# Kernel optimization log

Measured on AMD Instinct MI355X. Metric: run time of the kernel, lower is better.

The kernel has to match this reference:

```python
import jax, jax.numpy as jnp
import numpy as np

N = 100000   # nodes
E = 1600000  # edges (avg degree 16)
DIM = 128    # feature dim
EPS = 1e-6
NEG_SLOPE = 0.2  # tf.nn.leaky_relu default alpha


def layernorm(x, g, b):
    m = jnp.mean(x, axis=-1, keepdims=True)
    v = jnp.mean(jnp.square(x - m), axis=-1, keepdims=True)
    return g * (x - m) * jax.lax.rsqrt(v + EPS) + b


def setup_inputs() -> dict:
    key = jax.random.key(0)
    ks = jax.random.split(key, 12)
    s = 1.0 / np.sqrt(DIM)
    return {
        "query": jax.random.normal(ks[0], (N, DIM), jnp.float32),
        "adj_val": jax.random.uniform(ks[1], (E,), jnp.float32),
        "w_W": jax.random.normal(ks[2], (DIM, DIM), jnp.float32) * s,
        "w_b": jnp.zeros((DIM,), jnp.float32),
        "w1_W": jax.random.normal(ks[3], (DIM, DIM), jnp.float32) * s,
        "w1_b": jnp.zeros((DIM,), jnp.float32),
        "w2_W": jax.random.normal(ks[4], (DIM, DIM), jnp.float32) * s,
        "w2_b": jnp.zeros((DIM,), jnp.float32),
        "ln1_g": jnp.ones((DIM,), jnp.float32),
        "ln1_b": jnp.zeros((DIM,), jnp.float32),
        "ln2_g": jnp.ones((DIM,), jnp.float32),
        "ln2_b": jnp.zeros((DIM,), jnp.float32),
        "adj_row": jnp.sort(jax.random.randint(ks[5], (E,), 0, N, jnp.int32)),
        "adj_col": jax.random.randint(ks[6], (E,), 0, N, jnp.int32),
    }


def reference(query, adj_val, w_W, w_b, w1_W, w1_b, w2_W, w2_b,
              ln1_g, ln1_b, ln2_g, ln2_b, adj_row, adj_col):
    q = layernorm(query, ln1_g, ln1_b)          # [N, D]
    k = q                                        # key is None -> key = query
    value = k @ w_W + w_b                        # [N, D]

    # per-node scalar scores (mean_sum=False branch); dropout in eval mode (identity)
    sum1 = jnp.tanh(jnp.sum(q @ w1_W + w1_b, axis=1))   # [N]
    sum2 = jnp.tanh(jnp.sum(k @ w2_W + w2_b, axis=1))   # [N]

    # sparse add of col-scaled and row-scaled adjacency, then leaky_relu
    logits = jax.nn.leaky_relu(
        adj_val * sum1[adj_row] + adj_val * sum2[adj_col], NEG_SLOPE)  # [E]

    # sparse row-wise softmax over nonzeros
    row_max = jax.ops.segment_max(logits, adj_row, num_segments=N)
    ex = jnp.exp(logits - row_max[adj_row])
    row_sum = jax.ops.segment_sum(ex, adj_row, num_segments=N)
    attn = ex / row_sum[adj_row]                 # [E]

    # spmm: out[i] = sum_e attn[e] * value[col[e]]
    out = jax.ops.segment_sum(attn[:, None] * value[adj_col], adj_row,
                              num_segments=N)    # [N, D]
    return layernorm(out, ln2_g, ln2_b)
```

## Files before the change

### kernel.cpp

```cpp
#include <hip/hip_runtime.h>
#include <hip/hip_bf16.h>

typedef __attribute__((ext_vector_type(8))) short short8;
typedef __attribute__((ext_vector_type(8))) unsigned short ushort8;
typedef __attribute__((ext_vector_type(4))) float f32x4;
typedef __attribute__((ext_vector_type(2))) float f32x2;
typedef __attribute__((ext_vector_type(4))) unsigned int uint4v;

#define DIM 128
#define EPS 1e-6f

__device__ __forceinline__ float wave_sum(float v){
  #pragma unroll
  for (int m = 32; m >= 1; m >>= 1) v += __shfl_xor(v, m);
  return v;
}

__global__ void setup_kernel(const float* __restrict__ w_W,
                             const float* __restrict__ w1_W, const float* __restrict__ w1_b,
                             const float* __restrict__ w2_W, const float* __restrict__ w2_b,
                             __hip_bfloat16* __restrict__ wt_bf,
                             float* __restrict__ u1, float* __restrict__ u2,
                             float* __restrict__ c12){
  const int b = blockIdx.x, tid = threadIdx.x;
  if (b == 0){
    __shared__ float p1s[256], p2s[256];
    const int d = tid & 127, half = tid >> 7;
    const float4* w1p = (const float4*)(w1_W + d*DIM + half*64);
    const float4* w2p = (const float4*)(w2_W + d*DIM + half*64);
    float s1 = 0.f, s2 = 0.f;
    #pragma unroll 4
    for (int j = 0; j < 16; ++j){
      float4 a = w1p[j]; s1 += (a.x + a.y) + (a.z + a.w);
      float4 c = w2p[j]; s2 += (c.x + c.y) + (c.z + c.w);
    }
    p1s[tid] = s1; p2s[tid] = s2;
    __syncthreads();
    if (tid < 128){ u1[tid] = p1s[tid] + p1s[tid+128]; u2[tid] = p2s[tid] + p2s[tid+128]; }
    if (tid < 64){
      float c1 = w1_b[tid] + w1_b[tid + 64];
      float c2 = w2_b[tid] + w2_b[tid + 64];
      c1 = wave_sum(c1); c2 = wave_sum(c2);
      if (tid == 0){ c12[0] = c1; c12[1] = c2; }
    }
  } else {
    int idx = (b - 1) * 256 + tid;
    int j = idx >> 7, d = idx & 127;
    wt_bf[idx] = __float2bfloat16(w_W[d*DIM + j]);
  }
}

__launch_bounds__(256)
__global__ void node_kernel(const float* __restrict__ query,
                            const __hip_bfloat16* __restrict__ wt_bf,
                            const float* __restrict__ w_b,
                            const float* __restrict__ ln1_g, const float* __restrict__ ln1_b,
                            const float* __restrict__ u1, const float* __restrict__ u2,
                            const float* __restrict__ c12,
                            unsigned char* __restrict__ value_q,
                            float* __restrict__ sum1, float2* __restrict__ s2v, int N){
  __shared__ __hip_bfloat16 A[64][136];
  const int tid  = threadIdx.x;
  const int lane = tid & 63;
  const int w    = tid >> 6;
  const int q16  = lane >> 4;
  const int lq   = lane & 15;
  const int base = blockIdx.x * 64;

  float uu1[8], uu2[8], gg[8], bv[8];
  {
    const float* p1 = u1 + lq*8; const float* p2 = u2 + lq*8;
    const float* pg = ln1_g + lq*8; const float* pb = ln1_b + lq*8;
    #pragma unroll
    for (int j = 0; j < 8; ++j){ uu1[j]=p1[j]; uu2[j]=p2[j]; gg[j]=pg[j]; bv[j]=pb[j]; }
  }
  const float c1 = c12[0], c2 = c12[1];

  #pragma unroll
  for (int it = 0; it < 4; ++it){
    const int row = w*16 + it*4 + q16;
    const int n   = base + row;
    float x[8];
    if (n < N){
      const float4* qp = (const float4*)(query + (size_t)n*DIM + lq*8);
      float4 a = qp[0], b = qp[1];
      x[0]=a.x; x[1]=a.y; x[2]=a.z; x[3]=a.w;
      x[4]=b.x; x[5]=b.y; x[6]=b.z; x[7]=b.w;
    } else {
      #pragma unroll
      for (int j = 0; j < 8; ++j) x[j] = 0.f;
    }
    float s = 0.f, s2 = 0.f;
    #pragma unroll
    for (int j = 0; j < 8; ++j){ s += x[j]; s2 += x[j]*x[j]; }
    #pragma unroll
    for (int m = 1; m <= 8; m <<= 1){ s += __shfl_xor(s, m); s2 += __shfl_xor(s2, m); }
    const float mean = s * (1.f/128.f);
    const float var  = s2 * (1.f/128.f) - mean*mean;
    const float rs   = rsqrtf(var + EPS);

    float p1 = 0.f, p2 = 0.f;
    unsigned pk[4];
    #pragma unroll
    for (int j = 0; j < 4; ++j){
      float n0 = gg[2*j]   * (x[2*j]   - mean) * rs + bv[2*j];
      float n1 = gg[2*j+1] * (x[2*j+1] - mean) * rs + bv[2*j+1];
      p1 += n0*uu1[2*j] + n1*uu1[2*j+1];
      p2 += n0*uu2[2*j] + n1*uu2[2*j+1];
      union { __hip_bfloat16 h; unsigned short u; } a_, b_;
      a_.h = __float2bfloat16(n0); b_.h = __float2bfloat16(n1);
      pk[j] = ((unsigned)b_.u << 16) | (unsigned)a_.u;
    }
    uint4v pv = { pk[0], pk[1], pk[2], pk[3] };
    *(uint4v*)&A[row][lq*8] = pv;
    #pragma unroll
    for (int m = 1; m <= 8; m <<= 1){ p1 += __shfl_xor(p1, m); p2 += __shfl_xor(p2, m); }
    if (lq == 0 && n < N){
      sum1[n]   = tanhf(p1 + c1);
      s2v[n].x  = tanhf(p2 + c2);
    }
  }
  __syncthreads();

  const int rh = (w & 1) * 32;
  const int ch = (w >> 1) * 64;
  short8 afr[2][4];
  #pragma unroll
  for (int m = 0; m < 2; ++m)
    #pragma unroll
    for (int ks = 0; ks < 4; ++ks)
      afr[m][ks] = *(const short8*)&A[rh + m*16 + lq][ks*32 + q16*8];
  __syncthreads();

  #pragma unroll
  for (int jj = 0; jj < 4; ++jj){
    const int colb = ch + jj*16;
    f32x4 acc[2];
    acc[0] = (f32x4){0.f,0.f,0.f,0.f};
    acc[1] = (f32x4){0.f,0.f,0.f,0.f};
    #pragma unroll
    for (int ks = 0; ks < 4; ++ks){
      short8 bfr = *(const short8*)(wt_bf + (size_t)(colb + lq)*DIM + ks*32 + q16*8);
      acc[0] = __builtin_amdgcn_mfma_f32_16x16x32_bf16(afr[0][ks], bfr, acc[0], 0, 0, 0);
      acc[1] = __builtin_amdgcn_mfma_f32_16x16x32_bf16(afr[1][ks], bfr, acc[1], 0, 0, 0);
    }
    const int col  = colb + lq;
    const float bias = w_b[col];
    #pragma unroll
    for (int m = 0; m < 2; ++m)
      #pragma unroll
      for (int i = 0; i < 4; ++i)
        A[rh + m*16 + q16*4 + i][col] = __float2bfloat16(acc[m][i] + bias);
  }
  __syncthreads();

  const int row = tid >> 2, seg = tid & 3;
  const int n = base + row;
  float vals[32];
  float amax = 0.f;
  const ushort8* ap = (const ushort8*)&A[row][seg*32];
  #pragma unroll
  for (int h = 0; h < 4; ++h){
    ushort8 vv = ap[h];
    #pragma unroll
    for (int j = 0; j < 8; ++j){
      float f = __uint_as_float((unsigned)vv[j] << 16);
      vals[h*8 + j] = f;
      amax = fmaxf(amax, fabsf(f));
    }
  }
  amax = fmaxf(amax, __shfl_xor(amax, 1));
  amax = fmaxf(amax, __shfl_xor(amax, 2));
  const float qs = amax > 0.f ? 127.f / amax : 0.f;
  if (n < N){
    if (seg == 0) s2v[n].y = amax * (1.f/127.f);
    unsigned dw[8];
    #pragma unroll
    for (int d = 0; d < 8; ++d){
      unsigned q0 = (unsigned)__float2int_rn(fmaf(vals[4*d+0], qs, 128.f));
      unsigned q1 = (unsigned)__float2int_rn(fmaf(vals[4*d+1], qs, 128.f));
      unsigned q2 = (unsigned)__float2int_rn(fmaf(vals[4*d+2], qs, 128.f));
      unsigned q3 = (unsigned)__float2int_rn(fmaf(vals[4*d+3], qs, 128.f));
      dw[d] = q0 | (q1 << 8) | (q2 << 16) | (q3 << 24);
    }
    uint4v* dst = (uint4v*)(value_q + (size_t)n*DIM + seg*32);
    dst[0] = (uint4v){dw[0], dw[1], dw[2], dw[3]};
    dst[1] = (uint4v){dw[4], dw[5], dw[6], dw[7]};
  }
}

__global__ void pack_kernel(const float* __restrict__ adj_val, const int* __restrict__ adj_row,
                            const int* __restrict__ adj_col,
                            const float* __restrict__ sum1, const float2* __restrict__ s2v,
                            float2* __restrict__ excol, int* __restrict__ row_ptr,
                            int N, int E){
  int e = blockIdx.x * 256 + threadIdx.x;
  if (e >= E) return;
  int r  = adj_row[e];
  int rp = (e > 0) ? adj_row[e-1] : -1;
  if (rp != r){
    for (int rr = rp + 1; rr <= r; ++rr) row_ptr[rr] = e;
  }
  if (e == E - 1){
    for (int rr = r + 1; rr <= N; ++rr) row_ptr[rr] = E;
  }
  float av = adj_val[e];
  int c = adj_col[e];
  float2 sv = s2v[c];
  float x = av * (sum1[r] + sv.x);
  float lg = x > 0.f ? x : 0.2f * x;
  excol[e] = make_float2(__expf(lg) * sv.y, __int_as_float(c << 7));
}

__launch_bounds__(256)
__global__ void edge_kernel(const float2* __restrict__ excol, const int* __restrict__ row_ptr,
                            const unsigned char* __restrict__ value_q,
                            const float* __restrict__ ln2_g, const float* __restrict__ ln2_b,
                            float* __restrict__ out, int N){
  const int lane = threadIdx.x & 63;
  const int half = lane >> 5;
  const int ll   = lane & 31;
  const int q2   = ll >> 4;
  const int lq   = ll & 15;
  const int r = blockIdx.x * 8 + (threadIdx.x >> 6) * 2 + half;
  if (r >= N) return;
  const int2 rp = *(const int2*)(row_ptr + r);
  const int e0 = rp.x, e1 = rp.y;
  const unsigned char* vbase = value_q + lq*8;

  f32x2 acc2[4];
  #pragma unroll
  for (int j = 0; j < 4; ++j) acc2[j] = (f32x2){0.f, 0.f};

  int sb = e0;
  for (; sb + 8 <= e1; sb += 8){
    #pragma unroll
    for (int t = 0; t < 4; ++t){
      float2 ecv = excol[sb + q2 + t*2];
      const float wsc = ecv.x;
      const unsigned voff = (unsigned)__float_as_int(ecv.y);
      uint2 v = *(const uint2*)(vbase + voff);
      f32x2 w2 = { wsc, wsc };
      f32x2 p0 = { (float)( v.x        & 0xff), (float)((v.x >>  8) & 0xff) };
      f32x2 p1 = { (float)((v.x >> 16) & 0xff), (float)( v.x >> 24)         };
      f32x2 p2 = { (float)( v.y        & 0xff), (float)((v.y >>  8) & 0xff) };
      f32x2 p3 = { (float)((v.y >> 16) & 0xff), (float)( v.y >> 24)         };
      acc2[0] += w2 * p0;
      acc2[1] += w2 * p1;
      acc2[2] += w2 * p2;
      acc2[3] += w2 * p3;
    }
  }
  if (sb < e1){
    #pragma unroll
    for (int t = 0; t < 4; ++t){
      const int e = sb + q2 + t*2;
      float2 ecv = (e < e1) ? excol[e] : make_float2(0.f, 0.f);
      const float wsc = ecv.x;
      const unsigned voff = (unsigned)__float_as_int(ecv.y);
      uint2 v = *(const uint2*)(vbase + voff);
      f32x2 w2 = { wsc, wsc };
      f32x2 p0 = { (float)( v.x        & 0xff), (float)((v.x >>  8) & 0xff) };
      f32x2 p1 = { (float)((v.x >> 16) & 0xff), (float)( v.x >> 24)         };
      f32x2 p2 = { (float)( v.y        & 0xff), (float)((v.y >>  8) & 0xff) };
      f32x2 p3 = { (float)((v.y >> 16) & 0xff), (float)( v.y >> 24)         };
      acc2[0] += w2 * p0;
      acc2[1] += w2 * p1;
      acc2[2] += w2 * p2;
      acc2[3] += w2 * p3;
    }
  }

  #pragma unroll
  for (int j = 0; j < 4; ++j){
    acc2[j].x += __shfl_xor(acc2[j].x, 16);
    acc2[j].y += __shfl_xor(acc2[j].y, 16);
  }

  float sx = 0.f, sxx = 0.f;
  #pragma unroll
  for (int j = 0; j < 4; ++j){
    sx  += acc2[j].x + acc2[j].y;
    sxx += acc2[j].x*acc2[j].x + acc2[j].y*acc2[j].y;
  }
  #pragma unroll
  for (int m = 1; m <= 8; m <<= 1){ sx += __shfl_xor(sx, m); sxx += __shfl_xor(sxx, m); }
  const float mean = sx * (1.f/128.f);
  const float var  = sxx * (1.f/128.f) - mean*mean;
  const float rs   = rsqrtf(var + EPS);

  if (q2 == 0){
    float4 g0 = ((const float4*)ln2_g)[lq*2], g1 = ((const float4*)ln2_g)[lq*2+1];
    float4 b0 = ((const float4*)ln2_b)[lq*2], b1 = ((const float4*)ln2_b)[lq*2+1];
    float4 o0, o1;
    o0.x = g0.x*(acc2[0].x-mean)*rs + b0.x; o0.y = g0.y*(acc2[0].y-mean)*rs + b0.y;
    o0.z = g0.z*(acc2[1].x-mean)*rs + b0.z; o0.w = g0.w*(acc2[1].y-mean)*rs + b0.w;
    o1.x = g1.x*(acc2[2].x-mean)*rs + b1.x; o1.y = g1.y*(acc2[2].y-mean)*rs + b1.y;
    o1.z = g1.z*(acc2[3].x-mean)*rs + b1.z; o1.w = g1.w*(acc2[3].y-mean)*rs + b1.w;
    float4* op = (float4*)(out + (size_t)r*DIM + lq*8);
    op[0] = o0; op[1] = o1;
  }
}

extern "C" void kernel_launch(void* const* d_in, const int* in_sizes, int n_in,
                              void* d_out, int out_size, void* d_ws, size_t ws_size,
                              hipStream_t stream){
  const float* query   = (const float*)d_in[0];
  const float* adj_val = (const float*)d_in[1];
  const float* w_W     = (const float*)d_in[2];
  const float* w_b     = (const float*)d_in[3];
  const float* w1_W    = (const float*)d_in[4];
  const float* w1_b    = (const float*)d_in[5];
  const float* w2_W    = (const float*)d_in[6];
  const float* w2_b    = (const float*)d_in[7];
  const float* ln1_g   = (const float*)d_in[8];
  const float* ln1_b   = (const float*)d_in[9];
  const float* ln2_g   = (const float*)d_in[10];
  const float* ln2_b   = (const float*)d_in[11];
  const int*   adj_row = (const int*)d_in[12];
  const int*   adj_col = (const int*)d_in[13];

  const int N = in_sizes[0] / DIM;
  const int E = in_sizes[1];

  char* ws = (char*)d_ws;
  size_t off = 0;
  unsigned char* value_q = (unsigned char*)(ws + off); off += (size_t)N * DIM;
  float* sum1   = (float*)(ws + off); off += (size_t)N * 4;
  float2* s2v   = (float2*)(ws + off); off += (size_t)N * 8;
  int* row_ptr  = (int*)(ws + off);   off += (size_t)(N + 2) * 4;
  float* u1     = (float*)(ws + off); off += DIM * 4;
  float* u2     = (float*)(ws + off); off += DIM * 4;
  float* c12    = (float*)(ws + off); off += 2 * 4;
  off = (off + 63) & ~(size_t)63;
  __hip_bfloat16* wt_bf = (__hip_bfloat16*)(ws + off); off += DIM * DIM * 2;
  off = (off + 63) & ~(size_t)63;
  float2* excol = (float2*)(ws + off);

  setup_kernel<<<65, 256, 0, stream>>>(w_W, w1_W, w1_b, w2_W, w2_b, wt_bf, u1, u2, c12);
  node_kernel<<<(N + 63) / 64, 256, 0, stream>>>(query, wt_bf, w_b, ln1_g, ln1_b,
                                                 u1, u2, c12, value_q, sum1, s2v, N);
  pack_kernel<<<(E + 255) / 256, 256, 0, stream>>>(adj_val, adj_row, adj_col,
                                                   sum1, s2v, excol, row_ptr, N, E);
  edge_kernel<<<(N + 7) / 8, 256, 0, stream>>>(excol, row_ptr, value_q,
                                               ln2_g, ln2_b, (float*)d_out, N);
}
```

Before: 93.13 us.

## Fuse edge logit computation into SpMM kernel and build row_ptr by binary search

Removes the separate pack kernel and its intermediate excol array. Edge weights are now computed inside the edge kernel from adj_val, adj_col and the per-node scores. row_ptr is built in the setup kernel by a binary search over adj_row for each row. The change also splits the two tanh evaluations across two lanes and spreads the final LayerNorm stores over both half-waves. This saves one launch and an E-sized write-then-read round trip, at the cost of an extra dependent gather of s2v inside the SpMM loop and of recomputing exp there.

```diff
diff --git a/kernel.cpp b/kernel.cpp
--- a/kernel.cpp
+++ b/kernel.cpp
@@ -19,9 +19,11 @@
 __global__ void setup_kernel(const float* __restrict__ w_W,
                              const float* __restrict__ w1_W, const float* __restrict__ w1_b,
                              const float* __restrict__ w2_W, const float* __restrict__ w2_b,
+                             const int* __restrict__ adj_row,
                              __hip_bfloat16* __restrict__ wt_bf,
                              float* __restrict__ u1, float* __restrict__ u2,
-                             float* __restrict__ c12){
+                             float* __restrict__ c12,
+                             int* __restrict__ row_ptr, int N, int E){
   const int b = blockIdx.x, tid = threadIdx.x;
   if (b == 0){
     __shared__ float p1s[256], p2s[256];
@@ -43,10 +45,17 @@
       c1 = wave_sum(c1); c2 = wave_sum(c2);
       if (tid == 0){ c12[0] = c1; c12[1] = c2; }
     }
-  } else {
+  } else if (b <= 64){
     int idx = (b - 1) * 256 + tid;
     int j = idx >> 7, d = idx & 127;
     wt_bf[idx] = __float2bfloat16(w_W[d*DIM + j]);
+  } else {
+    int r = (b - 65) * 256 + tid;
+    if (r <= N){
+      int lo = 0, hi = E;
+      while (lo < hi){ int mid = (lo + hi) >> 1; if (adj_row[mid] < r) lo = mid + 1; else hi = mid; }
+      row_ptr[r] = lo;
+    }
   }
 }
 
@@ -115,9 +124,11 @@
     *(uint4v*)&A[row][lq*8] = pv;
     #pragma unroll
     for (int m = 1; m <= 8; m <<= 1){ p1 += __shfl_xor(p1, m); p2 += __shfl_xor(p2, m); }
-    if (lq == 0 && n < N){
-      sum1[n]   = tanhf(p1 + c1);
-      s2v[n].x  = tanhf(p2 + c2);
+    if (lq < 2 && n < N){
+      const float arg = (lq == 0) ? (p1 + c1) : (p2 + c2);
+      const float th = tanhf(arg);
+      if (lq == 0) sum1[n] = th;
+      else        s2v[n].x = th;
     }
   }
   __syncthreads();
@@ -189,34 +200,13 @@
   }
 }
 
-__global__ void pack_kernel(const float* __restrict__ adj_val, const int* __restrict__ adj_row,
-                            const int* __restrict__ adj_col,
+__launch_bounds__(256)
+__global__ void edge_kernel(const float* __restrict__ adj_val, const int* __restrict__ adj_col,
+                            const int* __restrict__ row_ptr,
                             const float* __restrict__ sum1, const float2* __restrict__ s2v,
-                            float2* __restrict__ excol, int* __restrict__ row_ptr,
-                            int N, int E){
-  int e = blockIdx.x * 256 + threadIdx.x;
-  if (e >= E) return;
-  int r  = adj_row[e];
-  int rp = (e > 0) ? adj_row[e-1] : -1;
-  if (rp != r){
-    for (int rr = rp + 1; rr <= r; ++rr) row_ptr[rr] = e;
-  }
-  if (e == E - 1){
-    for (int rr = r + 1; rr <= N; ++rr) row_ptr[rr] = E;
-  }
-  float av = adj_val[e];
-  int c = adj_col[e];
-  float2 sv = s2v[c];
-  float x = av * (sum1[r] + sv.x);
-  float lg = x > 0.f ? x : 0.2f * x;
-  excol[e] = make_float2(__expf(lg) * sv.y, __int_as_float(c << 7));
-}
-
-__launch_bounds__(256)
-__global__ void edge_kernel(const float2* __restrict__ excol, const int* __restrict__ row_ptr,
                             const unsigned char* __restrict__ value_q,
                             const float* __restrict__ ln2_g, const float* __restrict__ ln2_b,
-                            float* __restrict__ out, int N){
+                            float* __restrict__ out, int N, int E){
   const int lane = threadIdx.x & 63;
   const int half = lane >> 5;
   const int ll   = lane & 31;
@@ -226,6 +216,7 @@
   if (r >= N) return;
   const int2 rp = *(const int2*)(row_ptr + r);
   const int e0 = rp.x, e1 = rp.y;
+  const float s1r = sum1[r];
   const unsigned char* vbase = value_q + lq*8;
 
   f32x2 acc2[4];
@@ -236,10 +227,14 @@
   for (; sb + 8 <= e1; sb += 8){
     #pragma unroll
     for (int t = 0; t < 4; ++t){
-      float2 ecv = excol[sb + q2 + t*2];
-      const float wsc = ecv.x;
-      const unsigned voff = (unsigned)__float_as_int(ecv.y);
-      uint2 v = *(const uint2*)(vbase + voff);
+      const int e  = sb + q2 + t*2;
+      const float av = adj_val[e];
+      const int   ck = adj_col[e];
+      const float2 sv = s2v[ck];
+      uint2 v = *(const uint2*)(vbase + ((unsigned)ck << 7));
+      const float x   = av * (s1r + sv.x);
+      const float lg  = x > 0.f ? x : 0.2f * x;
+      const float wsc = __expf(lg) * sv.y;
       f32x2 w2 = { wsc, wsc };
       f32x2 p0 = { (float)( v.x        & 0xff), (float)((v.x >>  8) & 0xff) };
       f32x2 p1 = { (float)((v.x >> 16) & 0xff), (float)( v.x >> 24)         };
@@ -254,11 +249,15 @@
   if (sb < e1){
     #pragma unroll
     for (int t = 0; t < 4; ++t){
-      const int e = sb + q2 + t*2;
-      float2 ecv = (e < e1) ? excol[e] : make_float2(0.f, 0.f);
-      const float wsc = ecv.x;
-      const unsigned voff = (unsigned)__float_as_int(ecv.y);
-      uint2 v = *(const uint2*)(vbase + voff);
+      const int e  = sb + q2 + t*2;
+      const int ee = min(e, E - 1);
+      const float av = adj_val[ee];
+      const int   ck = adj_col[ee];
+      const float2 sv = s2v[ck];
+      uint2 v = *(const uint2*)(vbase + ((unsigned)ck << 7));
+      const float x   = av * (s1r + sv.x);
+      const float lg  = x > 0.f ? x : 0.2f * x;
+      const float wsc = (e < e1) ? __expf(lg) * sv.y : 0.f;
       f32x2 w2 = { wsc, wsc };
       f32x2 p0 = { (float)( v.x        & 0xff), (float)((v.x >>  8) & 0xff) };
       f32x2 p1 = { (float)((v.x >> 16) & 0xff), (float)( v.x >> 24)         };
@@ -283,23 +282,23 @@
     sx  += acc2[j].x + acc2[j].y;
     sxx += acc2[j].x*acc2[j].x + acc2[j].y*acc2[j].y;
   }
+  sx *= 0.5f; sxx *= 0.5f;
   #pragma unroll
   for (int m = 1; m <= 8; m <<= 1){ sx += __shfl_xor(sx, m); sxx += __shfl_xor(sxx, m); }
-  const float mean = sx * (1.f/128.f);
-  const float var  = sxx * (1.f/128.f) - mean*mean;
+  const float mean = sx * (2.f/128.f);
+  const float var  = sxx * (2.f/128.f) - mean*mean;
   const float rs   = rsqrtf(var + EPS);
 
-  if (q2 == 0){
-    float4 g0 = ((const float4*)ln2_g)[lq*2], g1 = ((const float4*)ln2_g)[lq*2+1];
-    float4 b0 = ((const float4*)ln2_b)[lq*2], b1 = ((const float4*)ln2_b)[lq*2+1];
-    float4 o0, o1;
-    o0.x = g0.x*(acc2[0].x-mean)*rs + b0.x; o0.y = g0.y*(acc2[0].y-mean)*rs + b0.y;
-    o0.z = g0.z*(acc2[1].x-mean)*rs + b0.z; o0.w = g0.w*(acc2[1].y-mean)*rs + b0.w;
-    o1.x = g1.x*(acc2[2].x-mean)*rs + b1.x; o1.y = g1.y*(acc2[2].y-mean)*rs + b1.y;
-    o1.z = g1.z*(acc2[3].x-mean)*rs + b1.z; o1.w = g1.w*(acc2[3].y-mean)*rs + b1.w;
-    float4* op = (float4*)(out + (size_t)r*DIM + lq*8);
-    op[0] = o0; op[1] = o1;
-  }
+  const float4 gq = ((const float4*)ln2_g)[lq*2 + q2];
+  const float4 bq = ((const float4*)ln2_b)[lq*2 + q2];
+  const f32x2 a0 = q2 ? acc2[2] : acc2[0];
+  const f32x2 a1 = q2 ? acc2[3] : acc2[1];
+  float4 o;
+  o.x = gq.x*(a0.x-mean)*rs + bq.x;
+  o.y = gq.y*(a0.y-mean)*rs + bq.y;
+  o.z = gq.z*(a1.x-mean)*rs + bq.z;
+  o.w = gq.w*(a1.y-mean)*rs + bq.w;
+  *(float4*)(out + (size_t)r*DIM + lq*8 + q2*4) = o;
 }
 
 extern "C" void kernel_launch(void* const* d_in, const int* in_sizes, int n_in,
@@ -333,15 +332,13 @@
   float* u2     = (float*)(ws + off); off += DIM * 4;
   float* c12    = (float*)(ws + off); off += 2 * 4;
   off = (off + 63) & ~(size_t)63;
-  __hip_bfloat16* wt_bf = (__hip_bfloat16*)(ws + off); off += DIM * DIM * 2;
-  off = (off + 63) & ~(size_t)63;
-  float2* excol = (float2*)(ws + off);
-
-  setup_kernel<<<65, 256, 0, stream>>>(w_W, w1_W, w1_b, w2_W, w2_b, wt_bf, u1, u2, c12);
+  __hip_bfloat16* wt_bf = (__hip_bfloat16*)(ws + off);
+
+  const int rp_blocks = (N + 1 + 255) / 256;
+  setup_kernel<<<65 + rp_blocks, 256, 0, stream>>>(w_W, w1_W, w1_b, w2_W, w2_b, adj_row,
+                                                   wt_bf, u1, u2, c12, row_ptr, N, E);
   node_kernel<<<(N + 63) / 64, 256, 0, stream>>>(query, wt_bf, w_b, ln1_g, ln1_b,
                                                  u1, u2, c12, value_q, sum1, s2v, N);
-  pack_kernel<<<(E + 255) / 256, 256, 0, stream>>>(adj_val, adj_row, adj_col,
-                                                   sum1, s2v, excol, row_ptr, N, E);
-  edge_kernel<<<(N + 7) / 8, 256, 0, stream>>>(excol, row_ptr, value_q,
-                                               ln2_g, ln2_b, (float*)d_out, N);
-}
+  edge_kernel<<<(N + 7) / 8, 256, 0, stream>>>(adj_val, adj_col, row_ptr, sum1, s2v,
+                                               value_q, ln2_g, ln2_b, (float*)d_out, N, E);
+}
```

Measured after the change: 101.4 us. +8.9%, slower.
